# Optimization experiments

Hardware: AMD Instinct MI355X
Metric: run time of the kernel (lower is better)

## Reference

```python
import jax, jax.numpy as jnp
import numpy as np

D_IN = 1024
D_OUT = 1024
NUM_HEADS = 16
HEAD_DIM = D_OUT // NUM_HEADS


def setup_inputs() -> dict:
    key = jax.random.key(0)
    k_x, k_q, k_k, k_v, k_o, k_ob = jax.random.split(key, 6)
    s_in = 1.0 / np.sqrt(D_IN)
    s_out = 1.0 / np.sqrt(D_OUT)
    return {
        "x": jax.random.normal(k_x, (4, 2048, D_IN), dtype=jnp.float32),
        "W_Q": jax.random.uniform(k_q, (D_IN, D_OUT), jnp.float32, -s_in, s_in),
        "W_K": jax.random.uniform(k_k, (D_IN, D_OUT), jnp.float32, -s_in, s_in),
        "W_V": jax.random.uniform(k_v, (D_IN, D_OUT), jnp.float32, -s_in, s_in),
        "W_O": jax.random.uniform(k_o, (D_OUT, D_OUT), jnp.float32, -s_out, s_out),
        "b_O": jax.random.uniform(k_ob, (D_OUT,), jnp.float32, -s_out, s_out),
    }


def reference(x, W_Q, W_K, W_V, W_O, b_O):
    B, T, _ = x.shape
    # projections -> [B, H, T, Dh]
    Q = (x @ W_Q).reshape(B, T, NUM_HEADS, HEAD_DIM).transpose(0, 2, 1, 3)
    K = (x @ W_K).reshape(B, T, NUM_HEADS, HEAD_DIM).transpose(0, 2, 1, 3)
    V = (x @ W_V).reshape(B, T, NUM_HEADS, HEAD_DIM).transpose(0, 2, 1, 3)
    scores = jnp.einsum("bhqd,bhkd->bhqk", Q, K) / np.sqrt(HEAD_DIM).astype(np.float32)
    causal = jnp.tril(jnp.ones((T, T), dtype=bool))  # True = keep
    scores = jnp.where(causal, scores, -jnp.inf)
    weights = jax.nn.softmax(scores, axis=-1)
    ctx = jnp.einsum("bhqk,bhkd->bhqd", weights, V)
    ctx = ctx.transpose(0, 2, 1, 3).reshape(B, T, D_OUT)
    return ctx @ W_O + b_O
```

## Files before the change

kernel.cpp:

```cpp
#include <hip/hip_runtime.h>

typedef unsigned short ushort_t;
typedef __attribute__((ext_vector_type(8))) __bf16 bf16x8;
typedef __attribute__((ext_vector_type(4))) float f32x4;
typedef __attribute__((ext_vector_type(16))) float f32x16;
typedef __attribute__((ext_vector_type(4))) unsigned short us4;
typedef __attribute__((ext_vector_type(8))) unsigned short us8;
typedef __attribute__((ext_vector_type(4))) unsigned int u32x4;

#define AS1 __attribute__((address_space(1)))
#define AS3 __attribute__((address_space(3)))

__device__ __forceinline__ unsigned short f2bf(float f) {
    unsigned u = __float_as_uint(f);
    u += 0x7fff + ((u >> 16) & 1);
    return (unsigned short)(u >> 16);
}

__device__ __forceinline__ unsigned cvtpk_bf16(float lo, float hi) {
    unsigned r;
    asm("v_cvt_pk_bf16_f32 %0, %1, %2" : "=v"(r) : "v"(lo), "v"(hi));
    return r;
}

__device__ __forceinline__ float fast_exp2(float x) {
    float r;
    asm("v_exp_f32 %0, %1" : "=v"(r) : "v"(x));
    return r;
}

__global__ void k_convert_x(const float* __restrict__ x, ushort_t* __restrict__ xb, int n4) {
    int i = blockIdx.x * blockDim.x + threadIdx.x;
    int stride = gridDim.x * blockDim.x;
    for (; i < n4; i += stride) {
        float4 f = reinterpret_cast<const float4*>(x)[i];
        us4 o = { f2bf(f.x), f2bf(f.y), f2bf(f.z), f2bf(f.w) };
        reinterpret_cast<us4*>(xb)[i] = o;
    }
}

__global__ void k_transpose_w(const float* __restrict__ wq, const float* __restrict__ wk,
                              const float* __restrict__ wv, const float* __restrict__ wo,
                              ushort_t* __restrict__ wqkvt, ushort_t* __restrict__ wot) {
    __shared__ float t[64][65];
    int bx = blockIdx.x;
    int w = bx >> 8;
    int ti = bx & 255;
    int k0 = (ti >> 4) * 64, n0 = (ti & 15) * 64;
    const float* src = (w == 0) ? wq : (w == 1) ? wk : (w == 2) ? wv : wo;
    ushort_t* dst = (w < 3) ? (wqkvt + (size_t)w * 1048576) : wot;
    for (int i = threadIdx.x; i < 4096; i += 256) {
        int r = i >> 6, c = i & 63;
        t[c][r] = src[(size_t)(k0 + r) * 1024 + n0 + c];
    }
    __syncthreads();
    for (int i = threadIdx.x; i < 4096; i += 256) {
        int r = i >> 6, c = i & 63;
        dst[(size_t)(n0 + r) * 1024 + k0 + c] = f2bf(t[r][c]);
    }
}

__global__ __launch_bounds__(512, 2) void k_gemm_qkv256(
    const ushort_t* __restrict__ A, const ushort_t* __restrict__ Bm,
    ushort_t* __restrict__ qd, ushort_t* __restrict__ kd, ushort_t* __restrict__ vd) {
    __shared__ __attribute__((aligned(16))) ushort_t lds[2 * 28672];

    const int tid = threadIdx.x, wid = tid >> 6, lane = tid & 63;
    const int lr = lane & 15, lg = lane >> 4;
    const int wm = wid >> 2, wn = wid & 3;

    int bid = blockIdx.x;
    int wg = (bid & 7) * 64 + (bid >> 3);
    const int by = wg >> 4, bx = wg & 15;
    const int row0 = by * 256, col0 = bx * 192;

    const int srcrow = lane >> 2;
    const int srccol = (((lane & 3) * 16) ^ ((lane >> 5) << 5)) >> 1;
    const ushort_t* aS = A  + (size_t)(row0 + srcrow) * 1024 + srccol;
    const ushort_t* bS = Bm + (size_t)(col0 + srcrow) * 1024 + srccol;
    const int rdoff = (lr * 64 + lg * 16) ^ ((lr >> 3) << 5);

    const int s0 = (wid & 3) + ((wid >> 2) << 3);
    const int s1 = s0 + 4;
    const int bmix_sr = 8 + (wid & 3);
    const int bmix_sc = wid >> 2;

#define STG_A(kt, sr, sc) \
    __builtin_amdgcn_global_load_lds((const AS1 void*)(aS + (size_t)(sr) * 16384 + (kt) * 64 + (sc) * 32), \
        (AS3 void*)((AS3 char*)lds + ((kt) & 1) * 57344 + (sr) * 2048 + (sc) * 1024), 16, 0, 0)
#define STG_B(kt, sr, sc) \
    __builtin_amdgcn_global_load_lds((const AS1 void*)(bS + (size_t)(sr) * 16384 + (kt) * 64 + (sc) * 32), \
        (AS3 void*)((AS3 char*)lds + ((kt) & 1) * 57344 + 32768 + (sr) * 2048 + (sc) * 1024), 16, 0, 0)
#define GRP1(kt)  { STG_A(kt, s0, 0); STG_B(kt, wid, 0); }
#define GRP2(kt)  { STG_A(kt, s1, 0); }
#define GRP3(kt)  { STG_A(kt, s0, 1); STG_B(kt, wid, 1); }
#define GTOP(kt)  { STG_A(kt, s1, 1); STG_B(kt, bmix_sr, bmix_sc); }

    f32x4 acc[8][3] = {};

    GRP1(0); GRP2(0); GRP3(0); GTOP(0);
    GRP1(1); GRP2(1); GRP3(1);

#pragma unroll 1
    for (int kt = 0; kt < 16; ++kt) {
        if (kt < 15) asm volatile("s_waitcnt vmcnt(5)" ::: "memory");
        else         asm volatile("s_waitcnt vmcnt(0)" ::: "memory");
        __builtin_amdgcn_s_barrier();
        if (kt < 15) GTOP(kt + 1);

        const char* bufA = (const char*)lds + (kt & 1) * 57344;
        const char* bufB = bufA + 32768;

        bf16x8 av0[4], av1[4], bv0[3], bv1[3];
#pragma unroll
        for (int x = 0; x < 4; ++x)
            av0[x] = *reinterpret_cast<const bf16x8*>(bufA + (wm * 8 + x) * 2048 + rdoff);
#pragma unroll
        for (int x = 0; x < 3; ++x)
            bv0[x] = *reinterpret_cast<const bf16x8*>(bufB + (wn * 3 + x) * 2048 + rdoff);

#pragma unroll
        for (int x = 0; x < 4; ++x)
            av1[x] = *reinterpret_cast<const bf16x8*>(bufA + (wm * 8 + 4 + x) * 2048 + rdoff);
        __builtin_amdgcn_s_setprio(1);
#pragma unroll
        for (int mf = 0; mf < 4; ++mf)
#pragma unroll
            for (int nf = 0; nf < 3; ++nf)
                acc[mf][nf] = __builtin_amdgcn_mfma_f32_16x16x32_bf16(av0[mf], bv0[nf], acc[mf][nf], 0, 0, 0);
        __builtin_amdgcn_s_setprio(0);
        __builtin_amdgcn_s_barrier();

#pragma unroll
        for (int x = 0; x < 4; ++x)
            av0[x] = *reinterpret_cast<const bf16x8*>(bufA + (wm * 8 + x) * 2048 + 1024 + rdoff);
#pragma unroll
        for (int x = 0; x < 3; ++x)
            bv1[x] = *reinterpret_cast<const bf16x8*>(bufB + (wn * 3 + x) * 2048 + 1024 + rdoff);
        __builtin_amdgcn_s_setprio(1);
#pragma unroll
        for (int mf = 0; mf < 4; ++mf)
#pragma unroll
            for (int nf = 0; nf < 3; ++nf)
                acc[4 + mf][nf] = __builtin_amdgcn_mfma_f32_16x16x32_bf16(av1[mf], bv0[nf], acc[4 + mf][nf], 0, 0, 0);
        __builtin_amdgcn_s_setprio(0);
        if (kt < 14) GRP1(kt + 2);
        __builtin_amdgcn_s_barrier();

#pragma unroll
        for (int x = 0; x < 4; ++x)
            av1[x] = *reinterpret_cast<const bf16x8*>(bufA + (wm * 8 + 4 + x) * 2048 + 1024 + rdoff);
        __builtin_amdgcn_s_setprio(1);
#pragma unroll
        for (int mf = 0; mf < 4; ++mf)
#pragma unroll
            for (int nf = 0; nf < 3; ++nf)
                acc[mf][nf] = __builtin_amdgcn_mfma_f32_16x16x32_bf16(av0[mf], bv1[nf], acc[mf][nf], 0, 0, 0);
        __builtin_amdgcn_s_setprio(0);
        if (kt < 14) GRP2(kt + 2);
        __builtin_amdgcn_s_barrier();

        __builtin_amdgcn_s_setprio(1);
#pragma unroll
        for (int mf = 0; mf < 4; ++mf)
#pragma unroll
            for (int nf = 0; nf < 3; ++nf)
                acc[4 + mf][nf] = __builtin_amdgcn_mfma_f32_16x16x32_bf16(av1[mf], bv1[nf], acc[4 + mf][nf], 0, 0, 0);
        __builtin_amdgcn_s_setprio(0);
        if (kt < 14) GRP3(kt + 2);
    }
#undef STG_A
#undef STG_B
#undef GRP1
#undef GRP2
#undef GRP3
#undef GTOP

#pragma unroll
    for (int mi = 0; mi < 8; ++mi) {
#pragma unroll
        for (int nf = 0; nf < 3; ++nf) {
            int col = col0 + wn * 48 + nf * 16 + lr;
            int w = col >> 10;
            int c1 = col & 1023;
            int h = c1 >> 6, dh = c1 & 63;
            ushort_t* dst = (w == 0) ? qd : (w == 1) ? kd : vd;
            const float osc = (w == 0) ? 0.18033688f : 1.0f;
#pragma unroll
            for (int e = 0; e < 4; ++e) {
                int row = row0 + wm * 128 + mi * 16 + lg * 4 + e;
                int b = row >> 11, t = row & 2047;
                dst[(((size_t)(b * 16 + h)) * 2048 + t) * 64 + dh] = f2bf(acc[mi][nf][e] * osc);
            }
        }
    }
}

__global__ __launch_bounds__(256) void k_transpose_v(const ushort_t* __restrict__ vd,
                                                     ushort_t* __restrict__ vt) {
    __shared__ __attribute__((aligned(16))) ushort_t tile[64 * 72];
    int bid = blockIdx.x;
    int bh = bid >> 5, tt = bid & 31;
    const ushort_t* src = vd + ((size_t)bh * 2048 + tt * 64) * 64;
    ushort_t* dst = vt + (size_t)bh * 2048 * 64 + tt * 64;
#pragma unroll
    for (int r = 0; r < 2; ++r) {
        int i = r * 256 + threadIdx.x;
        int t = i >> 3, c8 = (i & 7) * 8;
        us8 v = *reinterpret_cast<const us8*>(src + (size_t)t * 64 + c8);
        *reinterpret_cast<us8*>(&tile[t * 72 + (c8 ^ ((t >> 3) << 3))]) = v;
    }
    __syncthreads();
#pragma unroll
    for (int r = 0; r < 2; ++r) {
        int i = r * 256 + threadIdx.x;
        int dh = i >> 3, t8 = (i & 7) * 8;
        us8 o;
#pragma unroll
        for (int e = 0; e < 8; ++e)
            o[e] = tile[(t8 + e) * 72 + (dh ^ ((t8 >> 3) << 3))];
        *reinterpret_cast<us8*>(dst + (size_t)dh * 2048 + t8) = o;
    }
}

__global__ __launch_bounds__(256) void k_attn(
    const ushort_t* __restrict__ q, const ushort_t* __restrict__ k,
    const ushort_t* __restrict__ v, ushort_t* __restrict__ ctx) {
    __shared__ __attribute__((aligned(16))) ushort_t lsK[2 * 8192];
    __shared__ __attribute__((aligned(16))) ushort_t lsV[2 * 8192];

    const int tid = threadIdx.x, wid = tid >> 6, lane = tid & 63;
    const int l31 = lane & 31, hi = lane >> 5;
    const int bid = blockIdx.x;
    const int bh = bid & 63, pi = bid >> 6;
    const size_t base = (size_t)bh * 2048 * 64;
    const ushort_t* qg = q + base;
    const ushort_t* kg = k + base;
    const ushort_t* vtg = v + base;
    const int b = bh >> 4, h = bh & 15;

    const int skey = wid * 8 + (lane >> 3);
    const int scb0 = ((lane & 7) * 16) ^ ((skey & 7) << 4);
    const int kx = (l31 & 7) << 4;
    int koffA[4];
#pragma unroll
    for (int s = 0; s < 4; ++s)
        koffA[s] = l31 * 128 + ((s * 32 + hi * 16) ^ kx);

    us8 ow;
#pragma unroll
    for (int e = 0; e < 8; ++e) ow[e] = 0x3F80;
    const bf16x8 onef = __builtin_bit_cast(bf16x8, ow);

#pragma unroll 1
    for (int pass = 0; pass < 2; ++pass) {
        const int qt = pass ? pi : (15 - pi);
        const int q0 = qt * 128;
        const int q0w = q0 + wid * 32;
        const int qrow = q0w + l31;
        const int njt = qt + 1;

        bf16x8 qf[4];
#pragma unroll
        for (int s = 0; s < 4; ++s)
            qf[s] = *reinterpret_cast<const bf16x8*>(qg + (size_t)qrow * 64 + s * 16 + hi * 8);

        const ushort_t* kpr[4];
        const ushort_t* vpr[4];
#pragma unroll
        for (int r = 0; r < 4; ++r) {
            kpr[r] = kg + (size_t)(r * 32 + skey) * 64 + (scb0 >> 1);
            vpr[r] = vtg + (size_t)((r & 1) * 32 + skey) * 2048 + (r >> 1) * 64 + (scb0 >> 1);
        }

        f32x16 acc0 = {}, acc1 = {}, lacc = {};

        __syncthreads();
#pragma unroll
        for (int r = 0; r < 4; ++r) {
            __builtin_amdgcn_global_load_lds((const AS1 void*)kpr[r],
                (AS3 void*)((AS3 char*)lsK + r * 4096 + wid * 1024), 16, 0, 0);
            __builtin_amdgcn_global_load_lds((const AS1 void*)vpr[r],
                (AS3 void*)((AS3 char*)lsV + r * 4096 + wid * 1024), 16, 0, 0);
        }

        unsigned bo = 0;
        for (int jt = 0; jt < njt; ++jt) {
            __syncthreads();
            const int j0 = jt << 7;
            if (jt + 1 < njt) {
                const unsigned nb = bo ^ 16384;
#pragma unroll
                for (int r = 0; r < 4; ++r) {
                    kpr[r] += 8192;
                    vpr[r] += 128;
                    __builtin_amdgcn_global_load_lds((const AS1 void*)kpr[r],
                        (AS3 void*)((AS3 char*)lsK + nb + r * 4096 + wid * 1024), 16, 0, 0);
                    __builtin_amdgcn_global_load_lds((const AS1 void*)vpr[r],
                        (AS3 void*)((AS3 char*)lsV + nb + r * 4096 + wid * 1024), 16, 0, 0);
                }
            }

#pragma unroll
            for (int hh = 0; hh < 2; ++hh) {
                const int j0h = j0 + hh * 64;
                if (j0h < q0w + 32) {
                    const char* bK = reinterpret_cast<const char*>(lsK) + bo + hh * 8192;
                    const char* bV = reinterpret_cast<const char*>(lsV) + bo + hh * 8192;

                    f32x16 s0 = {}, s1 = {};
#pragma unroll
                    for (int s = 0; s < 4; ++s) {
                        bf16x8 ka = *reinterpret_cast<const bf16x8*>(bK + koffA[s]);
                        s0 = __builtin_amdgcn_mfma_f32_32x32x16_bf16(ka, qf[s], s0, 0, 0, 0);
                    }
#pragma unroll
                    for (int s = 0; s < 4; ++s) {
                        bf16x8 ka = *reinterpret_cast<const bf16x8*>(bK + 4096 + koffA[s]);
                        s1 = __builtin_amdgcn_mfma_f32_32x32x16_bf16(ka, qf[s], s1, 0, 0, 0);
                    }

                    float p0[16], p1[16];
                    if (j0h + 63 > q0w) {
                        const int jh = j0h + 4 * hi;
#pragma unroll
                        for (int r = 0; r < 16; ++r) {
                            const int kl = jh + (r & 3) + 8 * (r >> 2);
                            float e0 = fast_exp2(s0[r]);
                            float e1 = fast_exp2(s1[r]);
                            p0[r] = (kl > qrow) ? 0.f : e0;
                            p1[r] = (kl + 32 > qrow) ? 0.f : e1;
                        }
                    } else {
#pragma unroll
                        for (int r = 0; r < 16; ++r) {
                            p0[r] = fast_exp2(s0[r]);
                            p1[r] = fast_exp2(s1[r]);
                        }
                    }

#pragma unroll
                    for (int kb = 0; kb < 2; ++kb) {
                        const float* pp = kb ? p1 : p0;
                        unsigned pw[8];
#pragma unroll
                        for (int g = 0; g < 4; ++g) {
                            pw[2 * g]     = cvtpk_bf16(pp[4 * g],     pp[4 * g + 1]);
                            pw[2 * g + 1] = cvtpk_bf16(pp[4 * g + 2], pp[4 * g + 3]);
                        }
#pragma unroll
                        for (int j = 0; j < 2; ++j) {
                            asm("v_permlane32_swap_b32 %0, %1" : "+v"(pw[4 * j]),     "+v"(pw[4 * j + 2]));
                            asm("v_permlane32_swap_b32 %0, %1" : "+v"(pw[4 * j + 1]), "+v"(pw[4 * j + 3]));
                            u32x4 fw = { pw[4 * j], pw[4 * j + 1], pw[4 * j + 2], pw[4 * j + 3] };
                            bf16x8 pf = __builtin_bit_cast(bf16x8, fw);
                            const int jj = kb * 2 + j;
                            {
                                bf16x8 vf = *reinterpret_cast<const bf16x8*>(bV + koffA[jj]);
                                acc0 = __builtin_amdgcn_mfma_f32_32x32x16_bf16(vf, pf, acc0, 0, 0, 0);
                            }
                            {
                                bf16x8 vf = *reinterpret_cast<const bf16x8*>(bV + 4096 + koffA[jj]);
                                acc1 = __builtin_amdgcn_mfma_f32_32x32x16_bf16(vf, pf, acc1, 0, 0, 0);
                            }
                            lacc = __builtin_amdgcn_mfma_f32_32x32x16_bf16(onef, pf, lacc, 0, 0, 0);
                        }
                    }
                }
            }
            bo ^= 16384;
        }

        float inv = 1.0f / lacc[0];
        size_t orow = ((size_t)(b * 2048 + qrow)) * 1024 + h * 64;
#pragma unroll
        for (int g = 0; g < 4; ++g) {
            us4 o0 = { f2bf(acc0[4 * g] * inv),     f2bf(acc0[4 * g + 1] * inv),
                       f2bf(acc0[4 * g + 2] * inv), f2bf(acc0[4 * g + 3] * inv) };
            *reinterpret_cast<us4*>(&ctx[orow + 8 * g + 4 * hi]) = o0;
            us4 o1 = { f2bf(acc1[4 * g] * inv),     f2bf(acc1[4 * g + 1] * inv),
                       f2bf(acc1[4 * g + 2] * inv), f2bf(acc1[4 * g + 3] * inv) };
            *reinterpret_cast<us4*>(&ctx[orow + 32 + 8 * g + 4 * hi]) = o1;
        }
    }
}

__global__ __launch_bounds__(256, 2) void k_gemm_out(
    const ushort_t* __restrict__ cb, const ushort_t* __restrict__ wot,
    const float* __restrict__ bO, float* __restrict__ out) {
    __shared__ __attribute__((aligned(16))) ushort_t lds[2 * 16384];

    const int tid = threadIdx.x, wid = tid >> 6, lane = tid & 63;
    const int lr = lane & 15, lg = lane >> 4;
    const int wm = wid >> 1, wn = wid & 1;

    int bid = blockIdx.x;
    int wg = (bid & 7) * 64 + (bid >> 3);
    const int by = wg >> 3, bx = wg & 7;
    const int row0 = by * 128, col0 = bx * 128;

    const int srcrow = lane >> 2;
    const int srccol = (((lane & 3) * 16) ^ ((lane >> 5) << 5)) >> 1;
    const ushort_t* aS = cb  + (size_t)(row0 + srcrow) * 1024 + srccol;
    const ushort_t* bS = wot + (size_t)(col0 + srcrow) * 1024 + srccol;
    const int rdoff = (lr * 64 + lg * 16) ^ ((lr >> 3) << 5);

#define STG_A(kt, sr, sc) \
    __builtin_amdgcn_global_load_lds((const AS1 void*)(aS + (size_t)(sr) * 16384 + (kt) * 64 + (sc) * 32), \
        (AS3 void*)((AS3 char*)lds + ((kt) & 1) * 32768 + (sr) * 2048 + (sc) * 1024), 16, 0, 0)
#define STG_B(kt, sr, sc) \
    __builtin_amdgcn_global_load_lds((const AS1 void*)(bS + (size_t)(sr) * 16384 + (kt) * 64 + (sc) * 32), \
        (AS3 void*)((AS3 char*)lds + ((kt) & 1) * 32768 + 16384 + (sr) * 2048 + (sc) * 1024), 16, 0, 0)
#define GRP1(kt)  { STG_A(kt, wid, 0); STG_A(kt, wid + 4, 0); STG_B(kt, wid, 0); STG_B(kt, wid + 4, 0); }
#define GTOP(kt)  { STG_A(kt, wid, 1); STG_A(kt, wid + 4, 1); STG_B(kt, wid, 1); STG_B(kt, wid + 4, 1); }

    f32x4 acc[4][4] = {};

    GRP1(0); GTOP(0); GRP1(1);

#pragma unroll 1
    for (int kt = 0; kt < 16; ++kt) {
        if (kt < 15) asm volatile("s_waitcnt vmcnt(4)" ::: "memory");
        else         asm volatile("s_waitcnt vmcnt(0)" ::: "memory");
        __builtin_amdgcn_s_barrier();
        if (kt < 15) GTOP(kt + 1);

        const char* bufA = (const char*)lds + (kt & 1) * 32768;
        const char* bufB = bufA + 16384;

        bf16x8 av0[2], av1[2], bv0[4], bv1[4];
#pragma unroll
        for (int x = 0; x < 2; ++x)
            av0[x] = *reinterpret_cast<const bf16x8*>(bufA + (wm * 4 + x) * 2048 + rdoff);
#pragma unroll
        for (int x = 0; x < 4; ++x)
            bv0[x] = *reinterpret_cast<const bf16x8*>(bufB + (wn * 4 + x) * 2048 + rdoff);

#pragma unroll
        for (int x = 0; x < 2; ++x)
            av1[x] = *reinterpret_cast<const bf16x8*>(bufA + (wm * 4 + 2 + x) * 2048 + rdoff);
        __builtin_amdgcn_s_setprio(1);
#pragma unroll
        for (int mf = 0; mf < 2; ++mf)
#pragma unroll
            for (int nf = 0; nf < 4; ++nf)
                acc[mf][nf] = __builtin_amdgcn_mfma_f32_16x16x32_bf16(av0[mf], bv0[nf], acc[mf][nf], 0, 0, 0);
        __builtin_amdgcn_s_setprio(0);
        __builtin_amdgcn_s_barrier();

#pragma unroll
        for (int x = 0; x < 2; ++x)
            av0[x] = *reinterpret_cast<const bf16x8*>(bufA + (wm * 4 + x) * 2048 + 1024 + rdoff);
#pragma unroll
        for (int x = 0; x < 4; ++x)
            bv1[x] = *reinterpret_cast<const bf16x8*>(bufB + (wn * 4 + x) * 2048 + 1024 + rdoff);
        __builtin_amdgcn_s_setprio(1);
#pragma unroll
        for (int mf = 0; mf < 2; ++mf)
#pragma unroll
            for (int nf = 0; nf < 4; ++nf)
                acc[2 + mf][nf] = __builtin_amdgcn_mfma_f32_16x16x32_bf16(av1[mf], bv0[nf], acc[2 + mf][nf], 0, 0, 0);
        __builtin_amdgcn_s_setprio(0);
        if (kt < 14) GRP1(kt + 2);
        __builtin_amdgcn_s_barrier();

#pragma unroll
        for (int x = 0; x < 2; ++x)
            av1[x] = *reinterpret_cast<const bf16x8*>(bufA + (wm * 4 + 2 + x) * 2048 + 1024 + rdoff);
        __builtin_amdgcn_s_setprio(1);
#pragma unroll
        for (int mf = 0; mf < 2; ++mf)
#pragma unroll
            for (int nf = 0; nf < 4; ++nf)
                acc[mf][nf] = __builtin_amdgcn_mfma_f32_16x16x32_bf16(av0[mf], bv1[nf], acc[mf][nf], 0, 0, 0);
        __builtin_amdgcn_s_setprio(0);
        __builtin_amdgcn_s_barrier();

        __builtin_amdgcn_s_setprio(1);
#pragma unroll
        for (int mf = 0; mf < 2; ++mf)
#pragma unroll
            for (int nf = 0; nf < 4; ++nf)
                acc[2 + mf][nf] = __builtin_amdgcn_mfma_f32_16x16x32_bf16(av1[mf], bv1[nf], acc[2 + mf][nf], 0, 0, 0);
        __builtin_amdgcn_s_setprio(0);
    }
#undef STG_A
#undef STG_B
#undef GRP1
#undef GTOP

#pragma unroll
    for (int mf = 0; mf < 4; ++mf) {
#pragma unroll
        for (int nf = 0; nf < 4; ++nf) {
            int col = col0 + wn * 64 + nf * 16 + lr;
            float bias = bO[col];
#pragma unroll
            for (int e = 0; e < 4; ++e) {
                int row = row0 + wm * 64 + mf * 16 + lg * 4 + e;
                out[(size_t)row * 1024 + col] = acc[mf][nf][e] + bias;
            }
        }
    }
}

extern "C" void kernel_launch(void* const* d_in, const int* in_sizes, int n_in,
                              void* d_out, int out_size, void* d_ws, size_t ws_size,
                              hipStream_t stream) {
    const float* x  = (const float*)d_in[0];
    const float* wq = (const float*)d_in[1];
    const float* wk = (const float*)d_in[2];
    const float* wv = (const float*)d_in[3];
    const float* wo = (const float*)d_in[4];
    const float* bo = (const float*)d_in[5];
    float* out = (float*)d_out;

    char* ws = (char*)d_ws;
    ushort_t* xb    = (ushort_t*)(ws);
    ushort_t* wqkvt = (ushort_t*)(ws + 16777216);
    ushort_t* wot   = (ushort_t*)(ws + 23068672);
    ushort_t* qd    = (ushort_t*)(ws + 25165824);
    ushort_t* kd    = (ushort_t*)(ws + 41943040);
    ushort_t* vd    = (ushort_t*)(ws + 58720256);
    ushort_t* cd    = (ushort_t*)(ws + 75497472);
    ushort_t* vt    = xb;

    k_convert_x<<<2048, 256, 0, stream>>>(x, xb, 8192 * 1024 / 4);
    k_transpose_w<<<1024, 256, 0, stream>>>(wq, wk, wv, wo, wqkvt, wot);
    k_gemm_qkv256<<<512, 512, 0, stream>>>(xb, wqkvt, qd, kd, vd);
    k_transpose_v<<<2048, 256, 0, stream>>>(vd, vt);
    k_attn<<<512, 256, 0, stream>>>(qd, kd, vt, cd);
    k_gemm_out<<<dim3(512), 256, 0, stream>>>(cd, wot, bo, out);
}
```

Before: 156.8 us.

## Restructure attention into 256-row query tiles with 64-key stages

The attention kernel drops the two-pass paired query-tile scheme. Each block now handles one 256-row query tile, and each wave owns 64 query rows, so every K fragment loaded from LDS feeds two score MFMAs and every V fragment feeds two PV MFMAs. K/V staging shrinks to 64-key double-buffered tiles, halving LDS use, and launch bounds request 2 blocks per CU; s_setprio hints are added around the MFMA sections. The load balance across causal tiles changes from paired short/long tiles to one tile per block with higher-index tiles issued first, and register pressure rises from six accumulators.

```diff
diff --git a/kernel.cpp b/kernel.cpp
--- a/kernel.cpp
+++ b/kernel.cpp
@@ -223,24 +223,32 @@
     }
 }
 
-__global__ __launch_bounds__(256) void k_attn(
+__global__ __launch_bounds__(256, 2) void k_attn(
     const ushort_t* __restrict__ q, const ushort_t* __restrict__ k,
     const ushort_t* __restrict__ v, ushort_t* __restrict__ ctx) {
-    __shared__ __attribute__((aligned(16))) ushort_t lsK[2 * 8192];
-    __shared__ __attribute__((aligned(16))) ushort_t lsV[2 * 8192];
+    __shared__ __attribute__((aligned(16))) ushort_t lsK[2 * 4096];
+    __shared__ __attribute__((aligned(16))) ushort_t lsV[2 * 4096];
 
     const int tid = threadIdx.x, wid = tid >> 6, lane = tid & 63;
     const int l31 = lane & 31, hi = lane >> 5;
     const int bid = blockIdx.x;
-    const int bh = bid & 63, pi = bid >> 6;
+    const int bh = bid & 63, qt = 7 - (bid >> 6);
     const size_t base = (size_t)bh * 2048 * 64;
     const ushort_t* qg = q + base;
     const ushort_t* kg = k + base;
     const ushort_t* vtg = v + base;
     const int b = bh >> 4, h = bh & 15;
 
-    const int skey = wid * 8 + (lane >> 3);
-    const int scb0 = ((lane & 7) * 16) ^ ((skey & 7) << 4);
+    const int q0 = qt * 256;
+    const int q0w = q0 + wid * 64;
+    const int njt = 4 * qt + 4;
+    const int ntw = (q0w >> 6) + 1;
+
+    const int srow = tid >> 3;
+    const int ssw = ((((tid & 7) * 16) ^ ((srow & 7) << 4)) >> 1);
+    const ushort_t* kst = kg + (size_t)srow * 64 + ssw;
+    const ushort_t* vst = vtg + (size_t)srow * 2048 + ssw;
+
     const int kx = (l31 & 7) << 4;
     int koffA[4];
 #pragma unroll
@@ -252,135 +260,124 @@
     for (int e = 0; e < 8; ++e) ow[e] = 0x3F80;
     const bf16x8 onef = __builtin_bit_cast(bf16x8, ow);
 
+    bf16x8 qf[2][4];
+#pragma unroll
+    for (int qh = 0; qh < 2; ++qh)
+#pragma unroll
+        for (int s = 0; s < 4; ++s)
+            qf[qh][s] = *reinterpret_cast<const bf16x8*>(
+                qg + (size_t)(q0w + qh * 32 + l31) * 64 + s * 16 + hi * 8);
+
+    f32x16 acc00 = {}, acc01 = {}, acc10 = {}, acc11 = {}, lac0 = {}, lac1 = {};
+
+#define STAGE(bufb) {                                                                   \
+    __builtin_amdgcn_global_load_lds((const AS1 void*)kst,                              \
+        (AS3 void*)((AS3 char*)lsK + (bufb) + wid * 1024), 16, 0, 0);                   \
+    __builtin_amdgcn_global_load_lds((const AS1 void*)(kst + 2048),                     \
+        (AS3 void*)((AS3 char*)lsK + (bufb) + 4096 + wid * 1024), 16, 0, 0);            \
+    __builtin_amdgcn_global_load_lds((const AS1 void*)vst,                              \
+        (AS3 void*)((AS3 char*)lsV + (bufb) + wid * 1024), 16, 0, 0);                   \
+    __builtin_amdgcn_global_load_lds((const AS1 void*)(vst + 65536),                    \
+        (AS3 void*)((AS3 char*)lsV + (bufb) + 4096 + wid * 1024), 16, 0, 0);            \
+    kst += 4096; vst += 64; }
+
+    STAGE(0);
+
 #pragma unroll 1
-    for (int pass = 0; pass < 2; ++pass) {
-        const int qt = pass ? pi : (15 - pi);
-        const int q0 = qt * 128;
-        const int q0w = q0 + wid * 32;
-        const int qrow = q0w + l31;
-        const int njt = qt + 1;
-
-        bf16x8 qf[4];
-#pragma unroll
-        for (int s = 0; s < 4; ++s)
-            qf[s] = *reinterpret_cast<const bf16x8*>(qg + (size_t)qrow * 64 + s * 16 + hi * 8);
-
-        const ushort_t* kpr[4];
-        const ushort_t* vpr[4];
-#pragma unroll
-        for (int r = 0; r < 4; ++r) {
-            kpr[r] = kg + (size_t)(r * 32 + skey) * 64 + (scb0 >> 1);
-            vpr[r] = vtg + (size_t)((r & 1) * 32 + skey) * 2048 + (r >> 1) * 64 + (scb0 >> 1);
+    for (int t = 0; t < njt; ++t) {
+        __syncthreads();
+        const int bufc = (t & 1) * 8192;
+        if (t + 1 < njt) STAGE(((t + 1) & 1) * 8192);
+
+        if (t < ntw) {
+            const char* bK = reinterpret_cast<const char*>(lsK) + bufc;
+            const char* bV = reinterpret_cast<const char*>(lsV) + bufc;
+            const int j0 = t << 6;
+            const int rowA = q0w + l31, rowB = q0w + 32 + l31;
+
+#pragma unroll
+            for (int kh = 0; kh < 2; ++kh) {
+                f32x16 sA = {}, sB = {};
+                __builtin_amdgcn_s_setprio(1);
+#pragma unroll
+                for (int s = 0; s < 4; ++s) {
+                    bf16x8 kf = *reinterpret_cast<const bf16x8*>(bK + kh * 4096 + koffA[s]);
+                    sA = __builtin_amdgcn_mfma_f32_32x32x16_bf16(kf, qf[0][s], sA, 0, 0, 0);
+                    sB = __builtin_amdgcn_mfma_f32_32x32x16_bf16(kf, qf[1][s], sB, 0, 0, 0);
+                }
+                __builtin_amdgcn_s_setprio(0);
+
+                const int jh = j0 + kh * 32;
+                const bool nmA = (jh + 31 > q0w);
+                const bool nmB = (jh + 31 > q0w + 32);
+                float pA[16], pB[16];
+#pragma unroll
+                for (int r = 0; r < 16; ++r) {
+                    const int kl = jh + (r & 3) + 8 * (r >> 2) + 4 * hi;
+                    float eA = fast_exp2(sA[r]);
+                    float eB = fast_exp2(sB[r]);
+                    pA[r] = (nmA && kl > rowA) ? 0.f : eA;
+                    pB[r] = (nmB && kl > rowB) ? 0.f : eB;
+                }
+
+                unsigned pwA[8], pwB[8];
+#pragma unroll
+                for (int g = 0; g < 4; ++g) {
+                    pwA[2 * g]     = cvtpk_bf16(pA[4 * g],     pA[4 * g + 1]);
+                    pwA[2 * g + 1] = cvtpk_bf16(pA[4 * g + 2], pA[4 * g + 3]);
+                    pwB[2 * g]     = cvtpk_bf16(pB[4 * g],     pB[4 * g + 1]);
+                    pwB[2 * g + 1] = cvtpk_bf16(pB[4 * g + 2], pB[4 * g + 3]);
+                }
+                __builtin_amdgcn_s_setprio(1);
+#pragma unroll
+                for (int j2 = 0; j2 < 2; ++j2) {
+                    asm("v_permlane32_swap_b32 %0, %1" : "+v"(pwA[4 * j2]),     "+v"(pwA[4 * j2 + 2]));
+                    asm("v_permlane32_swap_b32 %0, %1" : "+v"(pwA[4 * j2 + 1]), "+v"(pwA[4 * j2 + 3]));
+                    asm("v_permlane32_swap_b32 %0, %1" : "+v"(pwB[4 * j2]),     "+v"(pwB[4 * j2 + 2]));
+                    asm("v_permlane32_swap_b32 %0, %1" : "+v"(pwB[4 * j2 + 1]), "+v"(pwB[4 * j2 + 3]));
+                    u32x4 fwA = { pwA[4 * j2], pwA[4 * j2 + 1], pwA[4 * j2 + 2], pwA[4 * j2 + 3] };
+                    u32x4 fwB = { pwB[4 * j2], pwB[4 * j2 + 1], pwB[4 * j2 + 2], pwB[4 * j2 + 3] };
+                    bf16x8 pfA = __builtin_bit_cast(bf16x8, fwA);
+                    bf16x8 pfB = __builtin_bit_cast(bf16x8, fwB);
+                    const int jj = kh * 2 + j2;
+                    {
+                        bf16x8 vf = *reinterpret_cast<const bf16x8*>(bV + koffA[jj]);
+                        acc00 = __builtin_amdgcn_mfma_f32_32x32x16_bf16(vf, pfA, acc00, 0, 0, 0);
+                        acc10 = __builtin_amdgcn_mfma_f32_32x32x16_bf16(vf, pfB, acc10, 0, 0, 0);
+                    }
+                    {
+                        bf16x8 vf = *reinterpret_cast<const bf16x8*>(bV + 4096 + koffA[jj]);
+                        acc01 = __builtin_amdgcn_mfma_f32_32x32x16_bf16(vf, pfA, acc01, 0, 0, 0);
+                        acc11 = __builtin_amdgcn_mfma_f32_32x32x16_bf16(vf, pfB, acc11, 0, 0, 0);
+                    }
+                    lac0 = __builtin_amdgcn_mfma_f32_32x32x16_bf16(onef, pfA, lac0, 0, 0, 0);
+                    lac1 = __builtin_amdgcn_mfma_f32_32x32x16_bf16(onef, pfB, lac1, 0, 0, 0);
+                }
+                __builtin_amdgcn_s_setprio(0);
+            }
         }
-
-        f32x16 acc0 = {}, acc1 = {}, lacc = {};
-
-        __syncthreads();
-#pragma unroll
-        for (int r = 0; r < 4; ++r) {
-            __builtin_amdgcn_global_load_lds((const AS1 void*)kpr[r],
-                (AS3 void*)((AS3 char*)lsK + r * 4096 + wid * 1024), 16, 0, 0);
-            __builtin_amdgcn_global_load_lds((const AS1 void*)vpr[r],
-                (AS3 void*)((AS3 char*)lsV + r * 4096 + wid * 1024), 16, 0, 0);
-        }
-
-        unsigned bo = 0;
-        for (int jt = 0; jt < njt; ++jt) {
-            __syncthreads();
-            const int j0 = jt << 7;
-            if (jt + 1 < njt) {
-                const unsigned nb = bo ^ 16384;
-#pragma unroll
-                for (int r = 0; r < 4; ++r) {
-                    kpr[r] += 8192;
-                    vpr[r] += 128;
-                    __builtin_amdgcn_global_load_lds((const AS1 void*)kpr[r],
-                        (AS3 void*)((AS3 char*)lsK + nb + r * 4096 + wid * 1024), 16, 0, 0);
-                    __builtin_amdgcn_global_load_lds((const AS1 void*)vpr[r],
-                        (AS3 void*)((AS3 char*)lsV + nb + r * 4096 + wid * 1024), 16, 0, 0);
-                }
-            }
-
-#pragma unroll
-            for (int hh = 0; hh < 2; ++hh) {
-                const int j0h = j0 + hh * 64;
-                if (j0h < q0w + 32) {
-                    const char* bK = reinterpret_cast<const char*>(lsK) + bo + hh * 8192;
-                    const char* bV = reinterpret_cast<const char*>(lsV) + bo + hh * 8192;
-
-                    f32x16 s0 = {}, s1 = {};
-#pragma unroll
-                    for (int s = 0; s < 4; ++s) {
-                        bf16x8 ka = *reinterpret_cast<const bf16x8*>(bK + koffA[s]);
-                        s0 = __builtin_amdgcn_mfma_f32_32x32x16_bf16(ka, qf[s], s0, 0, 0, 0);
-                    }
-#pragma unroll
-                    for (int s = 0; s < 4; ++s) {
-                        bf16x8 ka = *reinterpret_cast<const bf16x8*>(bK + 4096 + koffA[s]);
-                        s1 = __builtin_amdgcn_mfma_f32_32x32x16_bf16(ka, qf[s], s1, 0, 0, 0);
-                    }
-
-                    float p0[16], p1[16];
-                    if (j0h + 63 > q0w) {
-                        const int jh = j0h + 4 * hi;
-#pragma unroll
-                        for (int r = 0; r < 16; ++r) {
-                            const int kl = jh + (r & 3) + 8 * (r >> 2);
-                            float e0 = fast_exp2(s0[r]);
-                            float e1 = fast_exp2(s1[r]);
-                            p0[r] = (kl > qrow) ? 0.f : e0;
-                            p1[r] = (kl + 32 > qrow) ? 0.f : e1;
-                        }
-                    } else {
-#pragma unroll
-                        for (int r = 0; r < 16; ++r) {
-                            p0[r] = fast_exp2(s0[r]);
-                            p1[r] = fast_exp2(s1[r]);
-                        }
-                    }
-
-#pragma unroll
-                    for (int kb = 0; kb < 2; ++kb) {
-                        const float* pp = kb ? p1 : p0;
-                        unsigned pw[8];
-#pragma unroll
-                        for (int g = 0; g < 4; ++g) {
-                            pw[2 * g]     = cvtpk_bf16(pp[4 * g],     pp[4 * g + 1]);
-                            pw[2 * g + 1] = cvtpk_bf16(pp[4 * g + 2], pp[4 * g + 3]);
-                        }
-#pragma unroll
-                        for (int j = 0; j < 2; ++j) {
-                            asm("v_permlane32_swap_b32 %0, %1" : "+v"(pw[4 * j]),     "+v"(pw[4 * j + 2]));
-                            asm("v_permlane32_swap_b32 %0, %1" : "+v"(pw[4 * j + 1]), "+v"(pw[4 * j + 3]));
-                            u32x4 fw = { pw[4 * j], pw[4 * j + 1], pw[4 * j + 2], pw[4 * j + 3] };
-                            bf16x8 pf = __builtin_bit_cast(bf16x8, fw);
-                            const int jj = kb * 2 + j;
-                            {
-                                bf16x8 vf = *reinterpret_cast<const bf16x8*>(bV + koffA[jj]);
-                                acc0 = __builtin_amdgcn_mfma_f32_32x32x16_bf16(vf, pf, acc0, 0, 0, 0);
-                            }
-                            {
-                                bf16x8 vf = *reinterpret_cast<const bf16x8*>(bV + 4096 + koffA[jj]);
-                                acc1 = __builtin_amdgcn_mfma_f32_32x32x16_bf16(vf, pf, acc1, 0, 0, 0);
-                            }
-                            lacc = __builtin_amdgcn_mfma_f32_32x32x16_bf16(onef, pf, lacc, 0, 0, 0);
-                        }
-                    }
-                }
-            }
-            bo ^= 16384;
-        }
-
-        float inv = 1.0f / lacc[0];
-        size_t orow = ((size_t)(b * 2048 + qrow)) * 1024 + h * 64;
+    }
+#undef STAGE
+
+    {
+        float invA = 1.0f / lac0[0];
+        float invB = 1.0f / lac1[0];
+        size_t orowA = ((size_t)(b * 2048 + q0w + l31)) * 1024 + h * 64;
+        size_t orowB = ((size_t)(b * 2048 + q0w + 32 + l31)) * 1024 + h * 64;
 #pragma unroll
         for (int g = 0; g < 4; ++g) {
-            us4 o0 = { f2bf(acc0[4 * g] * inv),     f2bf(acc0[4 * g + 1] * inv),
-                       f2bf(acc0[4 * g + 2] * inv), f2bf(acc0[4 * g + 3] * inv) };
-            *reinterpret_cast<us4*>(&ctx[orow + 8 * g + 4 * hi]) = o0;
-            us4 o1 = { f2bf(acc1[4 * g] * inv),     f2bf(acc1[4 * g + 1] * inv),
-                       f2bf(acc1[4 * g + 2] * inv), f2bf(acc1[4 * g + 3] * inv) };
-            *reinterpret_cast<us4*>(&ctx[orow + 32 + 8 * g + 4 * hi]) = o1;
+            us4 oA0 = { f2bf(acc00[4 * g] * invA),     f2bf(acc00[4 * g + 1] * invA),
+                        f2bf(acc00[4 * g + 2] * invA), f2bf(acc00[4 * g + 3] * invA) };
+            *reinterpret_cast<us4*>(&ctx[orowA + 8 * g + 4 * hi]) = oA0;
+            us4 oA1 = { f2bf(acc01[4 * g] * invA),     f2bf(acc01[4 * g + 1] * invA),
+                        f2bf(acc01[4 * g + 2] * invA), f2bf(acc01[4 * g + 3] * invA) };
+            *reinterpret_cast<us4*>(&ctx[orowA + 32 + 8 * g + 4 * hi]) = oA1;
+            us4 oB0 = { f2bf(acc10[4 * g] * invB),     f2bf(acc10[4 * g + 1] * invB),
+                        f2bf(acc10[4 * g + 2] * invB), f2bf(acc10[4 * g + 3] * invB) };
+            *reinterpret_cast<us4*>(&ctx[orowB + 8 * g + 4 * hi]) = oB0;
+            us4 oB1 = { f2bf(acc11[4 * g] * invB),     f2bf(acc11[4 * g + 1] * invB),
+                        f2bf(acc11[4 * g + 2] * invB), f2bf(acc11[4 * g + 3] * invB) };
+            *reinterpret_cast<us4*>(&ctx[orowB + 32 + 8 * g + 4 * hi]) = oB1;
         }
     }
 }
```

New measurement: 186.8 us. 1.19x slower.

## Fuse paired causal query tiles into one pass sharing K/V loads

Applied to the files above, without the earlier changes.

The attention kernel used to process its two query tiles (15-pi and pi) in two sequential passes, each streaming K/V from global into LDS. Now both tiles are handled in one loop over the longer tile's key range, so every K/V fragment loaded to LDS and registers feeds both tiles' MFMAs, roughly halving K/V traffic and barriers. It also sets launch_bounds to 2 blocks per CU and adds s_setprio around MFMA sections. The cost is doubled accumulator and Q-fragment registers, which may cause spills under the tighter occupancy bound, plus more branching per 32-key chunk.

```diff
diff --git a/kernel.cpp b/kernel.cpp
--- a/kernel.cpp
+++ b/kernel.cpp
@@ -223,7 +223,7 @@
     }
 }
 
-__global__ __launch_bounds__(256) void k_attn(
+__global__ __launch_bounds__(256, 2) void k_attn(
     const ushort_t* __restrict__ q, const ushort_t* __restrict__ k,
     const ushort_t* __restrict__ v, ushort_t* __restrict__ ctx) {
     __shared__ __attribute__((aligned(16))) ushort_t lsK[2 * 8192];
@@ -233,12 +233,18 @@
     const int l31 = lane & 31, hi = lane >> 5;
     const int bid = blockIdx.x;
     const int bh = bid & 63, pi = bid >> 6;
+    const int qtA = 15 - pi, qtB = pi;
     const size_t base = (size_t)bh * 2048 * 64;
     const ushort_t* qg = q + base;
     const ushort_t* kg = k + base;
     const ushort_t* vtg = v + base;
     const int b = bh >> 4, h = bh & 15;
 
+    const int q0wA = qtA * 128 + wid * 32;
+    const int q0wB = qtB * 128 + wid * 32;
+    const int rowA = q0wA + l31, rowB = q0wB + l31;
+    const int njt = qtA + 1;
+
     const int skey = wid * 8 + (lane >> 3);
     const int scb0 = ((lane & 7) * 16) ^ ((skey & 7) << 4);
     const int kx = (l31 & 7) << 4;
@@ -252,135 +258,152 @@
     for (int e = 0; e < 8; ++e) ow[e] = 0x3F80;
     const bf16x8 onef = __builtin_bit_cast(bf16x8, ow);
 
+    bf16x8 qfA[4], qfB[4];
+#pragma unroll
+    for (int s = 0; s < 4; ++s) {
+        qfA[s] = *reinterpret_cast<const bf16x8*>(qg + (size_t)rowA * 64 + s * 16 + hi * 8);
+        qfB[s] = *reinterpret_cast<const bf16x8*>(qg + (size_t)rowB * 64 + s * 16 + hi * 8);
+    }
+
+    const ushort_t* kpr[4];
+    const ushort_t* vpr[4];
+#pragma unroll
+    for (int r = 0; r < 4; ++r) {
+        kpr[r] = kg + (size_t)(r * 32 + skey) * 64 + (scb0 >> 1);
+        vpr[r] = vtg + (size_t)((r & 1) * 32 + skey) * 2048 + (r >> 1) * 64 + (scb0 >> 1);
+    }
+
+    f32x16 aA0 = {}, aA1 = {}, aB0 = {}, aB1 = {}, lacA = {}, lacB = {};
+
+#pragma unroll
+    for (int r = 0; r < 4; ++r) {
+        __builtin_amdgcn_global_load_lds((const AS1 void*)kpr[r],
+            (AS3 void*)((AS3 char*)lsK + r * 4096 + wid * 1024), 16, 0, 0);
+        __builtin_amdgcn_global_load_lds((const AS1 void*)vpr[r],
+            (AS3 void*)((AS3 char*)lsV + r * 4096 + wid * 1024), 16, 0, 0);
+    }
+
+    unsigned bo = 0;
 #pragma unroll 1
-    for (int pass = 0; pass < 2; ++pass) {
-        const int qt = pass ? pi : (15 - pi);
-        const int q0 = qt * 128;
-        const int q0w = q0 + wid * 32;
-        const int qrow = q0w + l31;
-        const int njt = qt + 1;
-
-        bf16x8 qf[4];
-#pragma unroll
-        for (int s = 0; s < 4; ++s)
-            qf[s] = *reinterpret_cast<const bf16x8*>(qg + (size_t)qrow * 64 + s * 16 + hi * 8);
-
-        const ushort_t* kpr[4];
-        const ushort_t* vpr[4];
-#pragma unroll
-        for (int r = 0; r < 4; ++r) {
-            kpr[r] = kg + (size_t)(r * 32 + skey) * 64 + (scb0 >> 1);
-            vpr[r] = vtg + (size_t)((r & 1) * 32 + skey) * 2048 + (r >> 1) * 64 + (scb0 >> 1);
+    for (int jt = 0; jt < njt; ++jt) {
+        __syncthreads();
+        const int j0 = jt << 7;
+        if (jt + 1 < njt) {
+            const unsigned nb = bo ^ 16384;
+#pragma unroll
+            for (int r = 0; r < 4; ++r) {
+                kpr[r] += 8192;
+                vpr[r] += 128;
+                __builtin_amdgcn_global_load_lds((const AS1 void*)kpr[r],
+                    (AS3 void*)((AS3 char*)lsK + nb + r * 4096 + wid * 1024), 16, 0, 0);
+                __builtin_amdgcn_global_load_lds((const AS1 void*)vpr[r],
+                    (AS3 void*)((AS3 char*)lsV + nb + r * 4096 + wid * 1024), 16, 0, 0);
+            }
         }
 
-        f32x16 acc0 = {}, acc1 = {}, lacc = {};
-
-        __syncthreads();
-#pragma unroll
-        for (int r = 0; r < 4; ++r) {
-            __builtin_amdgcn_global_load_lds((const AS1 void*)kpr[r],
-                (AS3 void*)((AS3 char*)lsK + r * 4096 + wid * 1024), 16, 0, 0);
-            __builtin_amdgcn_global_load_lds((const AS1 void*)vpr[r],
-                (AS3 void*)((AS3 char*)lsV + r * 4096 + wid * 1024), 16, 0, 0);
-        }
-
-        unsigned bo = 0;
-        for (int jt = 0; jt < njt; ++jt) {
-            __syncthreads();
-            const int j0 = jt << 7;
-            if (jt + 1 < njt) {
-                const unsigned nb = bo ^ 16384;
-#pragma unroll
-                for (int r = 0; r < 4; ++r) {
-                    kpr[r] += 8192;
-                    vpr[r] += 128;
-                    __builtin_amdgcn_global_load_lds((const AS1 void*)kpr[r],
-                        (AS3 void*)((AS3 char*)lsK + nb + r * 4096 + wid * 1024), 16, 0, 0);
-                    __builtin_amdgcn_global_load_lds((const AS1 void*)vpr[r],
-                        (AS3 void*)((AS3 char*)lsV + nb + r * 4096 + wid * 1024), 16, 0, 0);
+#pragma unroll
+        for (int hh = 0; hh < 2; ++hh) {
+#pragma unroll
+            for (int kh = 0; kh < 2; ++kh) {
+                const int jh = j0 + hh * 64 + kh * 32;
+                const bool actA = jh < q0wA + 32;
+                const bool actB = jh < q0wB + 32;
+                if (actA) {
+                    const char* bK = reinterpret_cast<const char*>(lsK) + bo + hh * 8192 + kh * 4096;
+                    const char* bV = reinterpret_cast<const char*>(lsV) + bo + hh * 8192;
+
+                    f32x16 sA = {}, sB = {};
+                    __builtin_amdgcn_s_setprio(1);
+#pragma unroll
+                    for (int s = 0; s < 4; ++s) {
+                        bf16x8 kf = *reinterpret_cast<const bf16x8*>(bK + koffA[s]);
+                        sA = __builtin_amdgcn_mfma_f32_32x32x16_bf16(kf, qfA[s], sA, 0, 0, 0);
+                        if (actB)
+                            sB = __builtin_amdgcn_mfma_f32_32x32x16_bf16(kf, qfB[s], sB, 0, 0, 0);
+                    }
+                    __builtin_amdgcn_s_setprio(0);
+
+                    const bool nmA = (jh + 31 > q0wA);
+                    float pA[16], pB[16];
+#pragma unroll
+                    for (int r = 0; r < 16; ++r) {
+                        const int kl = jh + (r & 3) + 8 * (r >> 2) + 4 * hi;
+                        float eA = fast_exp2(sA[r]);
+                        pA[r] = (nmA && kl > rowA) ? 0.f : eA;
+                    }
+                    if (actB) {
+                        const bool nmB = (jh + 31 > q0wB);
+#pragma unroll
+                        for (int r = 0; r < 16; ++r) {
+                            const int kl = jh + (r & 3) + 8 * (r >> 2) + 4 * hi;
+                            float eB = fast_exp2(sB[r]);
+                            pB[r] = (nmB && kl > rowB) ? 0.f : eB;
+                        }
+                    }
+
+                    unsigned pwA[8], pwB[8];
+#pragma unroll
+                    for (int g = 0; g < 4; ++g) {
+                        pwA[2 * g]     = cvtpk_bf16(pA[4 * g],     pA[4 * g + 1]);
+                        pwA[2 * g + 1] = cvtpk_bf16(pA[4 * g + 2], pA[4 * g + 3]);
+                    }
+                    if (actB) {
+#pragma unroll
+                        for (int g = 0; g < 4; ++g) {
+                            pwB[2 * g]     = cvtpk_bf16(pB[4 * g],     pB[4 * g + 1]);
+                            pwB[2 * g + 1] = cvtpk_bf16(pB[4 * g + 2], pB[4 * g + 3]);
+                        }
+                    }
+
+                    __builtin_amdgcn_s_setprio(1);
+#pragma unroll
+                    for (int j2 = 0; j2 < 2; ++j2) {
+                        asm("v_permlane32_swap_b32 %0, %1" : "+v"(pwA[4 * j2]),     "+v"(pwA[4 * j2 + 2]));
+                        asm("v_permlane32_swap_b32 %0, %1" : "+v"(pwA[4 * j2 + 1]), "+v"(pwA[4 * j2 + 3]));
+                        u32x4 fwA = { pwA[4 * j2], pwA[4 * j2 + 1], pwA[4 * j2 + 2], pwA[4 * j2 + 3] };
+                        bf16x8 pfA = __builtin_bit_cast(bf16x8, fwA);
+                        const int jj = kh * 2 + j2;
+                        bf16x8 vf0 = *reinterpret_cast<const bf16x8*>(bV + koffA[jj]);
+                        bf16x8 vf1 = *reinterpret_cast<const bf16x8*>(bV + 4096 + koffA[jj]);
+                        aA0  = __builtin_amdgcn_mfma_f32_32x32x16_bf16(vf0, pfA, aA0, 0, 0, 0);
+                        aA1  = __builtin_amdgcn_mfma_f32_32x32x16_bf16(vf1, pfA, aA1, 0, 0, 0);
+                        lacA = __builtin_amdgcn_mfma_f32_32x32x16_bf16(onef, pfA, lacA, 0, 0, 0);
+                        if (actB) {
+                            asm("v_permlane32_swap_b32 %0, %1" : "+v"(pwB[4 * j2]),     "+v"(pwB[4 * j2 + 2]));
+                            asm("v_permlane32_swap_b32 %0, %1" : "+v"(pwB[4 * j2 + 1]), "+v"(pwB[4 * j2 + 3]));
+                            u32x4 fwB = { pwB[4 * j2], pwB[4 * j2 + 1], pwB[4 * j2 + 2], pwB[4 * j2 + 3] };
+                            bf16x8 pfB = __builtin_bit_cast(bf16x8, fwB);
+                            aB0  = __builtin_amdgcn_mfma_f32_32x32x16_bf16(vf0, pfB, aB0, 0, 0, 0);
+                            aB1  = __builtin_amdgcn_mfma_f32_32x32x16_bf16(vf1, pfB, aB1, 0, 0, 0);
+                            lacB = __builtin_amdgcn_mfma_f32_32x32x16_bf16(onef, pfB, lacB, 0, 0, 0);
+                        }
+                    }
+                    __builtin_amdgcn_s_setprio(0);
                 }
             }
-
-#pragma unroll
-            for (int hh = 0; hh < 2; ++hh) {
-                const int j0h = j0 + hh * 64;
-                if (j0h < q0w + 32) {
-                    const char* bK = reinterpret_cast<const char*>(lsK) + bo + hh * 8192;
-                    const char* bV = reinterpret_cast<const char*>(lsV) + bo + hh * 8192;
-
-                    f32x16 s0 = {}, s1 = {};
-#pragma unroll
-                    for (int s = 0; s < 4; ++s) {
-                        bf16x8 ka = *reinterpret_cast<const bf16x8*>(bK + koffA[s]);
-                        s0 = __builtin_amdgcn_mfma_f32_32x32x16_bf16(ka, qf[s], s0, 0, 0, 0);
-                    }
-#pragma unroll
-                    for (int s = 0; s < 4; ++s) {
-                        bf16x8 ka = *reinterpret_cast<const bf16x8*>(bK + 4096 + koffA[s]);
-                        s1 = __builtin_amdgcn_mfma_f32_32x32x16_bf16(ka, qf[s], s1, 0, 0, 0);
-                    }
-
-                    float p0[16], p1[16];
-                    if (j0h + 63 > q0w) {
-                        const int jh = j0h + 4 * hi;
-#pragma unroll
-                        for (int r = 0; r < 16; ++r) {
-                            const int kl = jh + (r & 3) + 8 * (r >> 2);
-                            float e0 = fast_exp2(s0[r]);
-                            float e1 = fast_exp2(s1[r]);
-                            p0[r] = (kl > qrow) ? 0.f : e0;
-                            p1[r] = (kl + 32 > qrow) ? 0.f : e1;
-                        }
-                    } else {
-#pragma unroll
-                        for (int r = 0; r < 16; ++r) {
-                            p0[r] = fast_exp2(s0[r]);
-                            p1[r] = fast_exp2(s1[r]);
-                        }
-                    }
-
-#pragma unroll
-                    for (int kb = 0; kb < 2; ++kb) {
-                        const float* pp = kb ? p1 : p0;
-                        unsigned pw[8];
-#pragma unroll
-                        for (int g = 0; g < 4; ++g) {
-                            pw[2 * g]     = cvtpk_bf16(pp[4 * g],     pp[4 * g + 1]);
-                            pw[2 * g + 1] = cvtpk_bf16(pp[4 * g + 2], pp[4 * g + 3]);
-                        }
-#pragma unroll
-                        for (int j = 0; j < 2; ++j) {
-                            asm("v_permlane32_swap_b32 %0, %1" : "+v"(pw[4 * j]),     "+v"(pw[4 * j + 2]));
-                            asm("v_permlane32_swap_b32 %0, %1" : "+v"(pw[4 * j + 1]), "+v"(pw[4 * j + 3]));
-                            u32x4 fw = { pw[4 * j], pw[4 * j + 1], pw[4 * j + 2], pw[4 * j + 3] };
-                            bf16x8 pf = __builtin_bit_cast(bf16x8, fw);
-                            const int jj = kb * 2 + j;
-                            {
-                                bf16x8 vf = *reinterpret_cast<const bf16x8*>(bV + koffA[jj]);
-                                acc0 = __builtin_amdgcn_mfma_f32_32x32x16_bf16(vf, pf, acc0, 0, 0, 0);
-                            }
-                            {
-                                bf16x8 vf = *reinterpret_cast<const bf16x8*>(bV + 4096 + koffA[jj]);
-                                acc1 = __builtin_amdgcn_mfma_f32_32x32x16_bf16(vf, pf, acc1, 0, 0, 0);
-                            }
-                            lacc = __builtin_amdgcn_mfma_f32_32x32x16_bf16(onef, pf, lacc, 0, 0, 0);
-                        }
-                    }
-                }
-            }
-            bo ^= 16384;
         }
-
-        float inv = 1.0f / lacc[0];
-        size_t orow = ((size_t)(b * 2048 + qrow)) * 1024 + h * 64;
+        bo ^= 16384;
+    }
+
+    {
+        float invA = 1.0f / lacA[0];
+        float invB = 1.0f / lacB[0];
+        size_t orowA = ((size_t)(b * 2048 + rowA)) * 1024 + h * 64;
+        size_t orowB = ((size_t)(b * 2048 + rowB)) * 1024 + h * 64;
 #pragma unroll
         for (int g = 0; g < 4; ++g) {
-            us4 o0 = { f2bf(acc0[4 * g] * inv),     f2bf(acc0[4 * g + 1] * inv),
-                       f2bf(acc0[4 * g + 2] * inv), f2bf(acc0[4 * g + 3] * inv) };
-            *reinterpret_cast<us4*>(&ctx[orow + 8 * g + 4 * hi]) = o0;
-            us4 o1 = { f2bf(acc1[4 * g] * inv),     f2bf(acc1[4 * g + 1] * inv),
-                       f2bf(acc1[4 * g + 2] * inv), f2bf(acc1[4 * g + 3] * inv) };
-            *reinterpret_cast<us4*>(&ctx[orow + 32 + 8 * g + 4 * hi]) = o1;
+            us4 oA0 = { f2bf(aA0[4 * g] * invA),     f2bf(aA0[4 * g + 1] * invA),
+                        f2bf(aA0[4 * g + 2] * invA), f2bf(aA0[4 * g + 3] * invA) };
+            *reinterpret_cast<us4*>(&ctx[orowA + 8 * g + 4 * hi]) = oA0;
+            us4 oA1 = { f2bf(aA1[4 * g] * invA),     f2bf(aA1[4 * g + 1] * invA),
+                        f2bf(aA1[4 * g + 2] * invA), f2bf(aA1[4 * g + 3] * invA) };
+            *reinterpret_cast<us4*>(&ctx[orowA + 32 + 8 * g + 4 * hi]) = oA1;
+            us4 oB0 = { f2bf(aB0[4 * g] * invB),     f2bf(aB0[4 * g + 1] * invB),
+                        f2bf(aB0[4 * g + 2] * invB), f2bf(aB0[4 * g + 3] * invB) };
+            *reinterpret_cast<us4*>(&ctx[orowB + 8 * g + 4 * hi]) = oB0;
+            us4 oB1 = { f2bf(aB1[4 * g] * invB),     f2bf(aB1[4 * g + 1] * invB),
+                        f2bf(aB1[4 * g + 2] * invB), f2bf(aB1[4 * g + 3] * invB) };
+            *reinterpret_cast<us4*>(&ctx[orowB + 32 + 8 * g + 4 * hi]) = oB1;
         }
     }
 }
```

After: 175.6 us. +12.0%, slower.
